# Kernel optimization log

Hardware: AMD Instinct MI355X
Metric: run time of the kernel (lower is better)

Reference implementation:

```python
import jax, jax.numpy as jnp
import numpy as np

B, T = 32, 512
IN, D, H, HD, L, FFN = 375, 512, 8, 64, 6, 1024
NC, CD, LAT, K = 4, 64, 256, 512
DL, DH, DFF, OUT = 4, 512, 1024, 291


def setup_inputs() -> dict:
    key = jax.random.key(0)
    ks = iter(jax.random.split(key, 64))
    def p(shape, scale=0.02):
        return jax.random.normal(next(ks), shape, jnp.float32) * scale
    return {
        "x": jax.random.normal(next(ks), (B, T, IN), jnp.float32),
        "in_w": p((IN, D)), "in_b": jnp.zeros((D,), jnp.float32),
        "enc_ln1_s": jnp.ones((L, D), jnp.float32), "enc_ln1_b": jnp.zeros((L, D), jnp.float32),
        "enc_qkv_w": p((L, D, 3 * D)), "enc_qkv_b": jnp.zeros((L, 3 * D), jnp.float32),
        "enc_out_w": p((L, D, D)), "enc_out_b": jnp.zeros((L, D), jnp.float32),
        "enc_ln2_s": jnp.ones((L, D), jnp.float32), "enc_ln2_b": jnp.zeros((L, D), jnp.float32),
        "enc_ff1_w": p((L, D, FFN)), "enc_ff1_b": jnp.zeros((L, FFN), jnp.float32),
        "enc_ff2_w": p((L, FFN, D)), "enc_ff2_b": jnp.zeros((L, D), jnp.float32),
        "lat_w": p((D, LAT)), "lat_b": jnp.zeros((LAT,), jnp.float32),
        "codebook": jax.random.uniform(next(ks), (K, CD), jnp.float32, -1.0 / K, 1.0 / K),
        "unlat_w": p((LAT, DH)), "unlat_b": jnp.zeros((DH,), jnp.float32),
        "dec_ln_s": jnp.ones((DL, DH), jnp.float32), "dec_ln_b": jnp.zeros((DL, DH), jnp.float32),
        "dec_ff1_w": p((DL, DH, DFF)), "dec_ff1_b": jnp.zeros((DL, DFF), jnp.float32),
        "dec_ff2_w": p((DL, DFF, DH)), "dec_ff2_b": jnp.zeros((DL, DH), jnp.float32),
        "out_w": p((DH, OUT)), "out_b": jnp.zeros((OUT,), jnp.float32),
    }


def _ln(x, s, b):
    m = x.mean(-1, keepdims=True)
    v = jnp.var(x, axis=-1, keepdims=True)
    return (x - m) / jnp.sqrt(v + 1e-5) * s + b


def _rope(x, cos, sin):
    # interleaved even/odd rotation, matches torch stack(...,-1).flatten(-2)
    xe, xo = x[..., 0::2], x[..., 1::2]
    re = xe * cos - xo * sin
    ro = xe * sin + xo * cos
    return jnp.stack((re, ro), axis=-1).reshape(x.shape)


def _forward(x, in_w, in_b, enc_ln1_s, enc_ln1_b, enc_qkv_w, enc_qkv_b,
             enc_out_w, enc_out_b, enc_ln2_s, enc_ln2_b, enc_ff1_w, enc_ff1_b,
             enc_ff2_w, enc_ff2_b, lat_w, lat_b, codebook, unlat_w, unlat_b,
             dec_ln_s, dec_ln_b, dec_ff1_w, dec_ff1_b, dec_ff2_w, dec_ff2_b,
             out_w, out_b):
    h = x @ in_w + in_b  # [B,T,D]
    inv_freq = 1.0 / (10000.0 ** (jnp.arange(0, HD, 2, dtype=jnp.float32) / HD))
    freqs = jnp.outer(jnp.arange(T, dtype=jnp.float32), inv_freq)  # [T, HD/2]
    cos, sin = jnp.cos(freqs), jnp.sin(freqs)
    for i in range(L):
        y = _ln(h, enc_ln1_s[i], enc_ln1_b[i])
        qkv = (y @ enc_qkv_w[i] + enc_qkv_b[i]).reshape(B, T, 3, H, HD)
        qkv = qkv.transpose(2, 0, 3, 1, 4)  # [3,B,H,T,HD]
        q, k, v = qkv[0], qkv[1], qkv[2]
        q = _rope(q, cos, sin)
        k = _rope(k, cos, sin)
        sc = jnp.einsum('bhqd,bhkd->bhqk', q, k) / np.float32(np.sqrt(HD))
        probs = jax.nn.softmax(sc, axis=-1)
        a = jnp.einsum('bhqk,bhkd->bhqd', probs, v)
        a = a.transpose(0, 2, 1, 3).reshape(B, T, D)
        h = h + (a @ enc_out_w[i] + enc_out_b[i])
        y = _ln(h, enc_ln2_s[i], enc_ln2_b[i])
        h = h + (jax.nn.gelu(y @ enc_ff1_w[i] + enc_ff1_b[i], approximate=False)
                 @ enc_ff2_w[i] + enc_ff2_b[i])
    # VQ bottleneck: split each token latent into NC subvectors, nearest code each
    z_bt = (h @ lat_w + lat_b).reshape(B * T, LAT)
    flat_z = z_bt.reshape(-1, CD)  # [B*T*NC, CD]
    d = ((flat_z ** 2).sum(1, keepdims=True)
         - 2.0 * (flat_z @ codebook.T)
         + (codebook ** 2).sum(1))  # [B*T*NC, K]
    idx = jnp.argmin(d, axis=1)
    q_bt = codebook[idx].reshape(B * T, LAT)
    st = z_bt + jax.lax.stop_gradient(q_bt - z_bt)  # straight-through
    g = st.reshape(B, T, LAT) @ unlat_w + unlat_b
    for i in range(DL):
        y = _ln(g, dec_ln_s[i], dec_ln_b[i])
        g = g + (jax.nn.gelu(y @ dec_ff1_w[i] + dec_ff1_b[i], approximate=False)
                 @ dec_ff2_w[i] + dec_ff2_b[i])
    return g @ out_w + out_b  # [B,T,291]


def reference(x, in_w, in_b, enc_ln1_s, enc_ln1_b, enc_qkv_w, enc_qkv_b,
              enc_out_w, enc_out_b, enc_ln2_s, enc_ln2_b, enc_ff1_w, enc_ff1_b,
              enc_ff2_w, enc_ff2_b, lat_w, lat_b, codebook, unlat_w, unlat_b,
              dec_ln_s, dec_ln_b, dec_ff1_w, dec_ff1_b, dec_ff2_w, dec_ff2_b,
              out_w, out_b):
    return _forward(x, in_w, in_b, enc_ln1_s, enc_ln1_b, enc_qkv_w, enc_qkv_b,
                    enc_out_w, enc_out_b, enc_ln2_s, enc_ln2_b, enc_ff1_w, enc_ff1_b,
                    enc_ff2_w, enc_ff2_b, lat_w, lat_b, codebook, unlat_w, unlat_b,
                    dec_ln_s, dec_ln_b, dec_ff1_w, dec_ff1_b, dec_ff2_w, dec_ff2_b,
                    out_w, out_b)
```

## Files before the change

### kernel.cpp

```cpp
#include <hip/hip_runtime.h>
#include <hip/hip_bf16.h>

#define BB 32
#define TT 512
#define IND 375
#define DD 512
#define HH 8
#define HDD 64
#define LL 6
#define FFNN 1024
#define LATD 256
#define KCODES 512
#define DLL 4
#define DHH 512
#define DFFF 1024
#define OUTD 291
#define MTOK (BB*TT)

__global__ void rope_table_k(float* __restrict__ cosb, float* __restrict__ sinb) {
  int idx = blockIdx.x * blockDim.x + threadIdx.x;
  if (idx >= TT * 32) return;
  int t = idx >> 5, i = idx & 31;
  float inv = powf(10000.0f, -(float)(2 * i) / 64.0f);
  float f = (float)t * inv;
  cosb[idx] = cosf(f);
  sinb[idx] = sinf(f);
}

template<int EPI>
__global__ __launch_bounds__(256) void gemm_k(const float* __restrict__ A,
                                              const float* __restrict__ W,
                                              const float* __restrict__ bias,
                                              const float* __restrict__ R,
                                              float* __restrict__ C,
                                              int M, int K, int N) {
  __shared__ float As[16][65];
  __shared__ float Bs[16][64];
  const int bn = blockIdx.x * 64;
  const int bm = blockIdx.y * 64;
  const int tid = threadIdx.x;
  const int tx = tid & 15, ty = tid >> 4;
  float acc[4][4] = {};

  for (int k0 = 0; k0 < K; k0 += 16) {
    {
      int r = tid >> 2, kk = (tid & 3) << 2;
      int gr = bm + r;
#pragma unroll
      for (int j = 0; j < 4; ++j) {
        int kg = k0 + kk + j;
        As[kk + j][r] = (gr < M && kg < K) ? A[(size_t)gr * K + kg] : 0.0f;
      }
    }
    {
      int kk = tid >> 4, nn = (tid & 15) << 2;
      int kg = k0 + kk;
#pragma unroll
      for (int j = 0; j < 4; ++j) {
        int ng = bn + nn + j;
        Bs[kk][nn + j] = (kg < K && ng < N) ? W[(size_t)kg * N + ng] : 0.0f;
      }
    }
    __syncthreads();
#pragma unroll
    for (int kk = 0; kk < 16; ++kk) {
      float a0[4], b0[4];
#pragma unroll
      for (int j = 0; j < 4; ++j) { a0[j] = As[kk][ty * 4 + j]; b0[j] = Bs[kk][tx * 4 + j]; }
#pragma unroll
      for (int ii = 0; ii < 4; ++ii)
#pragma unroll
        for (int jj = 0; jj < 4; ++jj)
          acc[ii][jj] += a0[ii] * b0[jj];
    }
    __syncthreads();
  }

#pragma unroll
  for (int ii = 0; ii < 4; ++ii) {
    int m = bm + ty * 4 + ii;
    if (m >= M) continue;
#pragma unroll
    for (int jj = 0; jj < 4; ++jj) {
      int n = bn + tx * 4 + jj;
      if (n >= N) continue;
      float v = acc[ii][jj] + bias[n];
      if (EPI == 1) v += R[(size_t)m * N + n];
      if (EPI == 2) v = 0.5f * v * (1.0f + erff(v * 0.70710678118654752f));
      C[(size_t)m * N + n] = v;
    }
  }
}

template<int EPI>
__global__ __launch_bounds__(256) void gemm128_k(const float* __restrict__ A,
                                                 const float* __restrict__ W,
                                                 const float* __restrict__ bias,
                                                 const float* __restrict__ R,
                                                 float* __restrict__ C,
                                                 int M, int K, int N) {
  __shared__ float As[16][128];
  __shared__ float4 Bs4[16][2][16];
  const int bn = blockIdx.x * 128;
  const int bm = blockIdx.y * 128;
  const int tid = threadIdx.x;
  const int tx = tid & 15;
  const int ty = tid >> 4;
  const int ar = tid >> 1;
  const int ak = (tid & 1) * 8;
  const int bk = tid >> 4;
  const int bx = tid & 15;

  float acc[8][8] = {};

  for (int k0 = 0; k0 < K; k0 += 16) {
    const float* ap = A + (size_t)(bm + ar) * K + k0 + ak;
    float4 a0 = *(const float4*)ap;
    float4 a1 = *(const float4*)(ap + 4);
    const float* bp = W + (size_t)(k0 + bk) * N + bn + bx * 8;
    float4 b0 = *(const float4*)bp;
    float4 b1 = *(const float4*)(bp + 4);

    __syncthreads();
    As[ak + 0][ar] = a0.x; As[ak + 1][ar] = a0.y; As[ak + 2][ar] = a0.z; As[ak + 3][ar] = a0.w;
    As[ak + 4][ar] = a1.x; As[ak + 5][ar] = a1.y; As[ak + 6][ar] = a1.z; As[ak + 7][ar] = a1.w;
    Bs4[bk][0][bx] = b0;
    Bs4[bk][1][bx] = b1;
    __syncthreads();

#pragma unroll
    for (int kk = 0; kk < 16; ++kk) {
      float4 va0 = *(const float4*)&As[kk][ty * 8];
      float4 va1 = *(const float4*)&As[kk][ty * 8 + 4];
      float4 vb0 = Bs4[kk][0][tx];
      float4 vb1 = Bs4[kk][1][tx];
      float av[8] = {va0.x, va0.y, va0.z, va0.w, va1.x, va1.y, va1.z, va1.w};
      float bv[8] = {vb0.x, vb0.y, vb0.z, vb0.w, vb1.x, vb1.y, vb1.z, vb1.w};
#pragma unroll
      for (int ii = 0; ii < 8; ++ii)
#pragma unroll
        for (int jj = 0; jj < 8; ++jj)
          acc[ii][jj] = __builtin_fmaf(av[ii], bv[jj], acc[ii][jj]);
    }
  }

#pragma unroll
  for (int ii = 0; ii < 8; ++ii) {
    int m = bm + ty * 8 + ii;
#pragma unroll
    for (int g = 0; g < 2; ++g) {
      int n0 = bn + tx * 8 + g * 4;
      float4 vv;
      float t[4];
#pragma unroll
      for (int j = 0; j < 4; ++j) {
        float v = acc[ii][g * 4 + j] + bias[n0 + j];
        if (EPI == 1) v += R[(size_t)m * N + n0 + j];
        if (EPI == 2) v = 0.5f * v * (1.0f + erff(v * 0.70710678118654752f));
        t[j] = v;
      }
      vv.x = t[0]; vv.y = t[1]; vv.z = t[2]; vv.w = t[3];
      *(float4*)&C[(size_t)m * N + n0] = vv;
    }
  }
}

__global__ __launch_bounds__(256) void ln_k(const float* __restrict__ X,
                                            const float* __restrict__ s,
                                            const float* __restrict__ b,
                                            float* __restrict__ Y) {
  int wave = threadIdx.x >> 6, lane = threadIdx.x & 63;
  int row = blockIdx.x * 4 + wave;
  const float* x = X + (size_t)row * DD;
  float v[8];
  float sum = 0.0f;
#pragma unroll
  for (int j = 0; j < 8; ++j) { v[j] = x[lane + 64 * j]; sum += v[j]; }
#pragma unroll
  for (int o = 32; o; o >>= 1) sum += __shfl_xor(sum, o);
  float mean = sum * (1.0f / 512.0f);
  float var = 0.0f;
#pragma unroll
  for (int j = 0; j < 8; ++j) { float d = v[j] - mean; var += d * d; }
#pragma unroll
  for (int o = 32; o; o >>= 1) var += __shfl_xor(var, o);
  float inv = 1.0f / sqrtf(var * (1.0f / 512.0f) + 1e-5f);
  float* y = Y + (size_t)row * DD;
#pragma unroll
  for (int j = 0; j < 8; ++j) {
    int d = lane + 64 * j;
    y[d] = (v[j] - mean) * inv * s[d] + b[d];
  }
}

__global__ void rope_k(float* __restrict__ qkv, const float* __restrict__ cosb,
                       const float* __restrict__ sinb) {
  int idx = blockIdx.x * blockDim.x + threadIdx.x;
  if (idx >= BB * TT * 2 * HH * 32) return;
  int i = idx & 31; idx >>= 5;
  int h = idx & 7;  idx >>= 3;
  int s = idx & 1;  idx >>= 1;
  int t = idx & 511; idx >>= 9;
  int b = idx;
  size_t base = ((size_t)(b * TT + t)) * (3 * DD) + s * DD + h * HDD + 2 * i;
  float c = cosb[t * 32 + i], sn = sinb[t * 32 + i];
  float xe = qkv[base], xo = qkv[base + 1];
  qkv[base]     = xe * c - xo * sn;
  qkv[base + 1] = xe * sn + xo * c;
}

__global__ __launch_bounds__(256) void fattn_k(const float* __restrict__ qkv,
                                               float* __restrict__ out) {
  __shared__ float Qs[64][68];
  __shared__ float KVs[64][68];
  __shared__ float Ps[64][68];
  const int tid = threadIdx.x;
  const int tx = tid & 15, ty = tid >> 4;
  const int qt = blockIdx.x & 7;
  const int h  = (blockIdx.x >> 3) & 7;
  const int b  = blockIdx.x >> 6;
  const float* base = qkv + (size_t)b * TT * (3 * DD) + h * HDD;

  {
    int r = tid & 63, q0 = tid >> 6;
#pragma unroll
    for (int jj = 0; jj < 4; ++jj) {
      int q = q0 + jj * 4;
      float4 v = *(const float4*)(base + (size_t)(qt * 64 + r) * (3 * DD) + q * 4);
      Qs[q * 4 + 0][r] = v.x; Qs[q * 4 + 1][r] = v.y;
      Qs[q * 4 + 2][r] = v.z; Qs[q * 4 + 3][r] = v.w;
    }
  }

  float o[4][4] = {};
  float m[4] = {-1e30f, -1e30f, -1e30f, -1e30f};
  float l[4] = {0.f, 0.f, 0.f, 0.f};

  for (int kt = 0; kt < 8; ++kt) {
    __syncthreads();
    {
      int r = tid & 63, q0 = tid >> 6;
#pragma unroll
      for (int jj = 0; jj < 4; ++jj) {
        int q = q0 + jj * 4;
        float4 v = *(const float4*)(base + (size_t)(kt * 64 + r) * (3 * DD) + DD + q * 4);
        KVs[q * 4 + 0][r] = v.x; KVs[q * 4 + 1][r] = v.y;
        KVs[q * 4 + 2][r] = v.z; KVs[q * 4 + 3][r] = v.w;
      }
    }
    __syncthreads();

    float s[4][4] = {};
#pragma unroll 4
    for (int d = 0; d < 64; ++d) {
      float4 a4 = *(const float4*)&Qs[d][ty * 4];
      float4 b4 = *(const float4*)&KVs[d][tx * 4];
      float av[4] = {a4.x, a4.y, a4.z, a4.w};
      float bv[4] = {b4.x, b4.y, b4.z, b4.w};
#pragma unroll
      for (int ii = 0; ii < 4; ++ii)
#pragma unroll
        for (int jj = 0; jj < 4; ++jj)
          s[ii][jj] = __builtin_fmaf(av[ii], bv[jj], s[ii][jj]);
    }

#pragma unroll
    for (int i = 0; i < 4; ++i) {
      float mm = fmaxf(fmaxf(s[i][0], s[i][1]), fmaxf(s[i][2], s[i][3])) * 0.125f;
#pragma unroll
      for (int off = 1; off < 16; off <<= 1) mm = fmaxf(mm, __shfl_xor(mm, off));
      float mn = fmaxf(m[i], mm);
      float f = expf(m[i] - mn);
      m[i] = mn;
      float ls = 0.0f;
#pragma unroll
      for (int j = 0; j < 4; ++j) {
        float p = expf(__builtin_fmaf(s[i][j], 0.125f, -mn));
        s[i][j] = p;
        ls += p;
      }
#pragma unroll
      for (int off = 1; off < 16; off <<= 1) ls += __shfl_xor(ls, off);
      l[i] = __builtin_fmaf(l[i], f, ls);
#pragma unroll
      for (int j = 0; j < 4; ++j) o[i][j] *= f;
    }

    __syncthreads();

#pragma unroll
    for (int j = 0; j < 4; ++j) {
      float4 pv; pv.x = s[0][j]; pv.y = s[1][j]; pv.z = s[2][j]; pv.w = s[3][j];
      *(float4*)&Ps[tx * 4 + j][ty * 4] = pv;
    }
#pragma unroll
    for (int ii = 0; ii < 4; ++ii) {
      int e = tid + 256 * ii;
      int c = e >> 4, q = e & 15;
      float4 v = *(const float4*)(base + (size_t)(kt * 64 + c) * (3 * DD) + 2 * DD + q * 4);
      *(float4*)&KVs[c][q * 4] = v;
    }
    __syncthreads();

#pragma unroll 4
    for (int c = 0; c < 64; ++c) {
      float4 a4 = *(const float4*)&Ps[c][ty * 4];
      float4 b4 = *(const float4*)&KVs[c][tx * 4];
      float av[4] = {a4.x, a4.y, a4.z, a4.w};
      float bv[4] = {b4.x, b4.y, b4.z, b4.w};
#pragma unroll
      for (int ii = 0; ii < 4; ++ii)
#pragma unroll
        for (int jj = 0; jj < 4; ++jj)
          o[ii][jj] = __builtin_fmaf(av[ii], bv[jj], o[ii][jj]);
    }
  }

#pragma unroll
  for (int i = 0; i < 4; ++i) {
    float inv = 1.0f / l[i];
    int tok = b * TT + qt * 64 + ty * 4 + i;
    float4 vv;
    vv.x = o[i][0] * inv; vv.y = o[i][1] * inv;
    vv.z = o[i][2] * inv; vv.w = o[i][3] * inv;
    *(float4*)&out[(size_t)tok * DD + h * HDD + tx * 4] = vv;
  }
}

__device__ __forceinline__ float npsumsq64(const float* __restrict__ a) {
  float r0 = __fmul_rn(a[0], a[0]), r1 = __fmul_rn(a[1], a[1]);
  float r2 = __fmul_rn(a[2], a[2]), r3 = __fmul_rn(a[3], a[3]);
  float r4 = __fmul_rn(a[4], a[4]), r5 = __fmul_rn(a[5], a[5]);
  float r6 = __fmul_rn(a[6], a[6]), r7 = __fmul_rn(a[7], a[7]);
#pragma unroll
  for (int i = 8; i < 64; i += 8) {
    r0 = __fadd_rn(r0, __fmul_rn(a[i + 0], a[i + 0]));
    r1 = __fadd_rn(r1, __fmul_rn(a[i + 1], a[i + 1]));
    r2 = __fadd_rn(r2, __fmul_rn(a[i + 2], a[i + 2]));
    r3 = __fadd_rn(r3, __fmul_rn(a[i + 3], a[i + 3]));
    r4 = __fadd_rn(r4, __fmul_rn(a[i + 4], a[i + 4]));
    r5 = __fadd_rn(r5, __fmul_rn(a[i + 5], a[i + 5]));
    r6 = __fadd_rn(r6, __fmul_rn(a[i + 6], a[i + 6]));
    r7 = __fadd_rn(r7, __fmul_rn(a[i + 7], a[i + 7]));
  }
  return __fadd_rn(__fadd_rn(__fadd_rn(r0, r1), __fadd_rn(r2, r3)),
                   __fadd_rn(__fadd_rn(r4, r5), __fadd_rn(r6, r7)));
}

__global__ void vqs2_k(const float* __restrict__ CB, float* __restrict__ S2) {
  int k = blockIdx.x * 256 + threadIdx.x;
  if (k < KCODES) S2[k] = npsumsq64(CB + (size_t)k * 64);
}

__global__ __launch_bounds__(256) void vq32b_k(const float* __restrict__ Z,
                                               const float* __restrict__ CB,
                                               const float* __restrict__ S2,
                                               int* __restrict__ idxOut) {
  __shared__ float zs[16][68];
  __shared__ float cs[64][68];
  __shared__ float s2s[64];
  __shared__ float rv[256];
  __shared__ int   ri[256];
  const int tid = threadIdx.x;
  const int lr = tid >> 4;
  const int sub = tid & 15;
  const int row0 = blockIdx.x * 16;

  {
    int r = tid >> 4, q = tid & 15;
    *(float4*)&zs[r][q * 4] = *(const float4*)(Z + (size_t)(row0 + r) * 64 + q * 4);
  }
  __syncthreads();

  const float S1 = npsumsq64(zs[lr]);

  float bv = 3.4e38f;
  int bi = 0x7fffffff;
  for (int ct = 0; ct < 8; ++ct) {
    __syncthreads();
    for (int e = tid; e < 1024; e += 256) {
      int r = e >> 4, q = e & 15;
      *(float4*)&cs[r][q * 4] = *(const float4*)(CB + (size_t)(ct * 64 + r) * 64 + q * 4);
    }
    if (tid < 64) s2s[tid] = S2[ct * 64 + tid];
    __syncthreads();
#pragma unroll
    for (int cc = 0; cc < 4; ++cc) {
      int kl = cc * 16 + sub;
      float g = 0.0f;
#pragma unroll
      for (int d4 = 0; d4 < 16; ++d4) {
        float4 zf = *(const float4*)&zs[lr][d4 * 4];
        float4 cf = *(const float4*)&cs[kl][d4 * 4];
        g = __builtin_fmaf(zf.x, cf.x, g);
        g = __builtin_fmaf(zf.y, cf.y, g);
        g = __builtin_fmaf(zf.z, cf.z, g);
        g = __builtin_fmaf(zf.w, cf.w, g);
      }
      float d32 = __fadd_rn(__fsub_rn(S1, __fmul_rn(2.0f, g)), s2s[kl]);
      int k = ct * 64 + kl;
      if (d32 < bv || (d32 == bv && k < bi)) { bv = d32; bi = k; }
    }
  }
  rv[tid] = bv; ri[tid] = bi;
  __syncthreads();
  if (sub == 0) {
    float bb = rv[tid]; int ii = ri[tid];
#pragma unroll
    for (int j = 1; j < 16; ++j) {
      float v = rv[tid + j]; int id = ri[tid + j];
      if (v < bb || (v == bb && id < ii)) { bb = v; ii = id; }
    }
    idxOut[row0 + lr] = ii;
  }
}

__global__ void stgather_k(const float* __restrict__ Z, const float* __restrict__ CB,
                           const int* __restrict__ idx, float* __restrict__ Q) {
  int e = blockIdx.x * blockDim.x + threadIdx.x;
  if (e >= MTOK * LATD) return;
  int chunk = e >> 6, d = e & 63;
  int k = idx[chunk] & (KCODES - 1);
  float z = Z[e];
  float c = CB[(size_t)k * 64 + d];
  Q[e] = __fadd_rn(z, __fsub_rn(c, z));
}

static inline dim3 gemm_grid(int M, int N) { return dim3((N + 63) / 64, (M + 63) / 64); }
static inline dim3 g128(int M, int N) { return dim3(N / 128, M / 128); }

extern "C" void kernel_launch(void* const* d_in, const int* in_sizes, int n_in,
                              void* d_out, int out_size, void* d_ws, size_t ws_size,
                              hipStream_t stream) {
  const float* x        = (const float*)d_in[0];
  const float* in_w     = (const float*)d_in[1];
  const float* in_b     = (const float*)d_in[2];
  const float* ln1_s    = (const float*)d_in[3];
  const float* ln1_b    = (const float*)d_in[4];
  const float* qkv_w    = (const float*)d_in[5];
  const float* qkv_b    = (const float*)d_in[6];
  const float* aout_w   = (const float*)d_in[7];
  const float* aout_b   = (const float*)d_in[8];
  const float* ln2_s    = (const float*)d_in[9];
  const float* ln2_b    = (const float*)d_in[10];
  const float* ff1_w    = (const float*)d_in[11];
  const float* ff1_b    = (const float*)d_in[12];
  const float* ff2_w    = (const float*)d_in[13];
  const float* ff2_b    = (const float*)d_in[14];
  const float* lat_w    = (const float*)d_in[15];
  const float* lat_b    = (const float*)d_in[16];
  const float* codebook = (const float*)d_in[17];
  const float* unlat_w  = (const float*)d_in[18];
  const float* unlat_b  = (const float*)d_in[19];
  const float* dln_s    = (const float*)d_in[20];
  const float* dln_b    = (const float*)d_in[21];
  const float* dff1_w   = (const float*)d_in[22];
  const float* dff1_b   = (const float*)d_in[23];
  const float* dff2_w   = (const float*)d_in[24];
  const float* dff2_b   = (const float*)d_in[25];
  const float* ow       = (const float*)d_in[26];
  const float* ob       = (const float*)d_in[27];
  float* out = (float*)d_out;

  float* ws   = (float*)d_ws;
  float* Hb   = ws;
  float* Yb   = Hb + (size_t)MTOK * DD;
  float* QKVb = Yb + (size_t)MTOK * DD;
  float* COSb = QKVb + (size_t)MTOK * 3 * DD;
  float* SINb = COSb + TT * 32;
  int*   IDXb = (int*)(SINb + TT * 32);
  float* S2b  = (float*)(IDXb + MTOK * 4);

  dim3 blk(256);

  rope_table_k<<<(TT * 32 + 255) / 256, blk, 0, stream>>>(COSb, SINb);
  vqs2_k<<<2, blk, 0, stream>>>(codebook, S2b);

  gemm_k<0><<<gemm_grid(MTOK, DD), blk, 0, stream>>>(x, in_w, in_b, nullptr, Hb, MTOK, IND, DD);

  for (int l = 0; l < LL; ++l) {
    ln_k<<<MTOK / 4, blk, 0, stream>>>(Hb, ln1_s + l * DD, ln1_b + l * DD, Yb);
    gemm128_k<0><<<g128(MTOK, 3 * DD), blk, 0, stream>>>(Yb, qkv_w + (size_t)l * DD * 3 * DD,
                                                         qkv_b + l * 3 * DD, nullptr, QKVb,
                                                         MTOK, DD, 3 * DD);
    rope_k<<<(BB * TT * 2 * HH * 32) / 256, blk, 0, stream>>>(QKVb, COSb, SINb);
    fattn_k<<<BB * HH * (TT / 64), blk, 0, stream>>>(QKVb, Yb);
    gemm128_k<1><<<g128(MTOK, DD), blk, 0, stream>>>(Yb, aout_w + (size_t)l * DD * DD,
                                                     aout_b + l * DD, Hb, Hb, MTOK, DD, DD);
    ln_k<<<MTOK / 4, blk, 0, stream>>>(Hb, ln2_s + l * DD, ln2_b + l * DD, Yb);
    gemm128_k<2><<<g128(MTOK, FFNN), blk, 0, stream>>>(Yb, ff1_w + (size_t)l * DD * FFNN,
                                                       ff1_b + l * FFNN, nullptr, QKVb,
                                                       MTOK, DD, FFNN);
    gemm128_k<1><<<g128(MTOK, DD), blk, 0, stream>>>(QKVb, ff2_w + (size_t)l * FFNN * DD,
                                                     ff2_b + l * DD, Hb, Hb, MTOK, FFNN, DD);
  }

  gemm128_k<0><<<g128(MTOK, LATD), blk, 0, stream>>>(Hb, lat_w, lat_b, nullptr, Yb, MTOK, DD, LATD);
  vq32b_k<<<(MTOK * 4) / 16, blk, 0, stream>>>(Yb, codebook, S2b, IDXb);
  stgather_k<<<(MTOK * LATD) / 256, blk, 0, stream>>>(Yb, codebook, IDXb, QKVb);
  gemm128_k<0><<<g128(MTOK, DHH), blk, 0, stream>>>(QKVb, unlat_w, unlat_b, nullptr, Hb, MTOK, LATD, DHH);

  for (int l = 0; l < DLL; ++l) {
    ln_k<<<MTOK / 4, blk, 0, stream>>>(Hb, dln_s + l * DHH, dln_b + l * DHH, Yb);
    gemm128_k<2><<<g128(MTOK, DFFF), blk, 0, stream>>>(Yb, dff1_w + (size_t)l * DHH * DFFF,
                                                       dff1_b + l * DFFF, nullptr, QKVb,
                                                       MTOK, DHH, DFFF);
    gemm128_k<1><<<g128(MTOK, DHH), blk, 0, stream>>>(QKVb, dff2_w + (size_t)l * DFFF * DHH,
                                                      dff2_b + l * DHH, Hb, Hb, MTOK, DFFF, DHH);
  }

  gemm_k<0><<<gemm_grid(MTOK, OUTD), blk, 0, stream>>>(Hb, ow, ob, nullptr, out, MTOK, DD, OUTD);
}
```

Before: 9.342 ms.

## Double-buffer GEMM tiles, fuse RoPE into QKV epilogue, XCD-aware block swizzle

The main fp32 GEMM now double-buffers its shared-memory tiles, prefetching the next K-slice into registers while computing the current one, and uses one sync per step instead of two. It also remaps blocks to a 1D grid with XCD-aware swizzling for L2 locality. RoPE is fused into the QKV GEMM epilogue, removing a separate read-modify-write pass over Q and K. The small 64x64 GEMM used for the ragged input and output projections is replaced by a guarded 128x128 variant. Attention block indexing is remapped so that blocks landing on the same XCD share batch and head. The cost is doubled shared memory per block, which may lower occupancy.

```diff
diff --git a/kernel.cpp b/kernel.cpp
--- a/kernel.cpp
+++ b/kernel.cpp
@@ -28,106 +28,146 @@
 }
 
 template<int EPI>
-__global__ __launch_bounds__(256) void gemm_k(const float* __restrict__ A,
-                                              const float* __restrict__ W,
-                                              const float* __restrict__ bias,
-                                              const float* __restrict__ R,
-                                              float* __restrict__ C,
-                                              int M, int K, int N) {
-  __shared__ float As[16][65];
-  __shared__ float Bs[16][64];
-  const int bn = blockIdx.x * 64;
-  const int bm = blockIdx.y * 64;
-  const int tid = threadIdx.x;
-  const int tx = tid & 15, ty = tid >> 4;
-  float acc[4][4] = {};
-
-  for (int k0 = 0; k0 < K; k0 += 16) {
-    {
-      int r = tid >> 2, kk = (tid & 3) << 2;
-      int gr = bm + r;
-#pragma unroll
-      for (int j = 0; j < 4; ++j) {
-        int kg = k0 + kk + j;
-        As[kk + j][r] = (gr < M && kg < K) ? A[(size_t)gr * K + kg] : 0.0f;
-      }
-    }
-    {
-      int kk = tid >> 4, nn = (tid & 15) << 2;
-      int kg = k0 + kk;
-#pragma unroll
-      for (int j = 0; j < 4; ++j) {
-        int ng = bn + nn + j;
-        Bs[kk][nn + j] = (kg < K && ng < N) ? W[(size_t)kg * N + ng] : 0.0f;
-      }
-    }
-    __syncthreads();
-#pragma unroll
-    for (int kk = 0; kk < 16; ++kk) {
-      float a0[4], b0[4];
-#pragma unroll
-      for (int j = 0; j < 4; ++j) { a0[j] = As[kk][ty * 4 + j]; b0[j] = Bs[kk][tx * 4 + j]; }
-#pragma unroll
-      for (int ii = 0; ii < 4; ++ii)
-#pragma unroll
-        for (int jj = 0; jj < 4; ++jj)
-          acc[ii][jj] += a0[ii] * b0[jj];
-    }
-    __syncthreads();
-  }
-
-#pragma unroll
-  for (int ii = 0; ii < 4; ++ii) {
-    int m = bm + ty * 4 + ii;
-    if (m >= M) continue;
-#pragma unroll
-    for (int jj = 0; jj < 4; ++jj) {
-      int n = bn + tx * 4 + jj;
-      if (n >= N) continue;
-      float v = acc[ii][jj] + bias[n];
-      if (EPI == 1) v += R[(size_t)m * N + n];
-      if (EPI == 2) v = 0.5f * v * (1.0f + erff(v * 0.70710678118654752f));
-      C[(size_t)m * N + n] = v;
-    }
-  }
-}
-
-template<int EPI>
 __global__ __launch_bounds__(256) void gemm128_k(const float* __restrict__ A,
                                                  const float* __restrict__ W,
                                                  const float* __restrict__ bias,
                                                  const float* __restrict__ R,
                                                  float* __restrict__ C,
-                                                 int M, int K, int N) {
+                                                 int M, int K, int N,
+                                                 const float* __restrict__ COS,
+                                                 const float* __restrict__ SIN) {
+  __shared__ float As[2][16][128];
+  __shared__ float4 Bs4[2][16][2][16];
+  const int nbx = N >> 7;
+  const int per = gridDim.x >> 3;
+  const int bid = blockIdx.x;
+  const int lin = (bid & 7) * per + (bid >> 3);
+  const int by = lin / nbx, bx = lin - by * nbx;
+  const int bn = bx * 128, bm = by * 128;
+  const int tid = threadIdx.x;
+  const int tx = tid & 15, ty = tid >> 4;
+  const int ar = tid >> 1, ak = (tid & 1) * 8;
+  const int bk = tid >> 4, bxs = tid & 15;
+
+  const float* ap0 = A + (size_t)(bm + ar) * K + ak;
+  const float* bp0 = W + (size_t)bk * N + bn + bxs * 8;
+
+  float acc[8][8] = {};
+  float4 a0, a1, b0, b1;
+
+  a0 = *(const float4*)ap0;
+  a1 = *(const float4*)(ap0 + 4);
+  b0 = *(const float4*)bp0;
+  b1 = *(const float4*)(bp0 + 4);
+  As[0][ak + 0][ar] = a0.x; As[0][ak + 1][ar] = a0.y; As[0][ak + 2][ar] = a0.z; As[0][ak + 3][ar] = a0.w;
+  As[0][ak + 4][ar] = a1.x; As[0][ak + 5][ar] = a1.y; As[0][ak + 6][ar] = a1.z; As[0][ak + 7][ar] = a1.w;
+  Bs4[0][bk][0][bxs] = b0;
+  Bs4[0][bk][1][bxs] = b1;
+  __syncthreads();
+
+  const int nt = K >> 4;
+  int cur = 0;
+  for (int t = 0; t < nt; ++t) {
+    if (t + 1 < nt) {
+      const float* ap = ap0 + (t + 1) * 16;
+      a0 = *(const float4*)ap;
+      a1 = *(const float4*)(ap + 4);
+      const float* bp = bp0 + (size_t)(t + 1) * 16 * N;
+      b0 = *(const float4*)bp;
+      b1 = *(const float4*)(bp + 4);
+    }
+#pragma unroll
+    for (int kk = 0; kk < 16; ++kk) {
+      float4 va0 = *(const float4*)&As[cur][kk][ty * 8];
+      float4 va1 = *(const float4*)&As[cur][kk][ty * 8 + 4];
+      float4 vb0 = Bs4[cur][kk][0][tx];
+      float4 vb1 = Bs4[cur][kk][1][tx];
+      float av[8] = {va0.x, va0.y, va0.z, va0.w, va1.x, va1.y, va1.z, va1.w};
+      float bv[8] = {vb0.x, vb0.y, vb0.z, vb0.w, vb1.x, vb1.y, vb1.z, vb1.w};
+#pragma unroll
+      for (int ii = 0; ii < 8; ++ii)
+#pragma unroll
+        for (int jj = 0; jj < 8; ++jj)
+          acc[ii][jj] = __builtin_fmaf(av[ii], bv[jj], acc[ii][jj]);
+    }
+    if (t + 1 < nt) {
+      int nx = cur ^ 1;
+      As[nx][ak + 0][ar] = a0.x; As[nx][ak + 1][ar] = a0.y; As[nx][ak + 2][ar] = a0.z; As[nx][ak + 3][ar] = a0.w;
+      As[nx][ak + 4][ar] = a1.x; As[nx][ak + 5][ar] = a1.y; As[nx][ak + 6][ar] = a1.z; As[nx][ak + 7][ar] = a1.w;
+      Bs4[nx][bk][0][bxs] = b0;
+      Bs4[nx][bk][1][bxs] = b1;
+      __syncthreads();
+      cur = nx;
+    }
+  }
+
+#pragma unroll
+  for (int ii = 0; ii < 8; ++ii) {
+    int m = bm + ty * 8 + ii;
+#pragma unroll
+    for (int g = 0; g < 2; ++g) {
+      int n0 = bn + tx * 8 + g * 4;
+      float t4[4];
+#pragma unroll
+      for (int j = 0; j < 4; ++j) {
+        float v = acc[ii][g * 4 + j] + bias[n0 + j];
+        if (EPI == 1) v += R[(size_t)m * N + n0 + j];
+        if (EPI == 2) v = 0.5f * v * (1.0f + erff(v * 0.70710678118654752f));
+        t4[j] = v;
+      }
+      if (EPI == 3 && n0 < 2 * DD) {
+        int tpos = m & 511;
+        int i0 = (n0 & 63) >> 1;
+        float c0 = COS[tpos * 32 + i0],     s0 = SIN[tpos * 32 + i0];
+        float c1 = COS[tpos * 32 + i0 + 1], s1 = SIN[tpos * 32 + i0 + 1];
+        float xe0 = t4[0], xo0 = t4[1], xe1 = t4[2], xo1 = t4[3];
+        t4[0] = xe0 * c0 - xo0 * s0;
+        t4[1] = xe0 * s0 + xo0 * c0;
+        t4[2] = xe1 * c1 - xo1 * s1;
+        t4[3] = xe1 * s1 + xo1 * c1;
+      }
+      float4 vv; vv.x = t4[0]; vv.y = t4[1]; vv.z = t4[2]; vv.w = t4[3];
+      *(float4*)&C[(size_t)m * N + n0] = vv;
+    }
+  }
+}
+
+template<int EPI>
+__global__ __launch_bounds__(256) void gemm128g_k(const float* __restrict__ A,
+                                                  const float* __restrict__ W,
+                                                  const float* __restrict__ bias,
+                                                  const float* __restrict__ R,
+                                                  float* __restrict__ C,
+                                                  int M, int K, int N) {
   __shared__ float As[16][128];
   __shared__ float4 Bs4[16][2][16];
   const int bn = blockIdx.x * 128;
   const int bm = blockIdx.y * 128;
   const int tid = threadIdx.x;
-  const int tx = tid & 15;
-  const int ty = tid >> 4;
-  const int ar = tid >> 1;
-  const int ak = (tid & 1) * 8;
-  const int bk = tid >> 4;
-  const int bx = tid & 15;
-
+  const int tx = tid & 15, ty = tid >> 4;
   float acc[8][8] = {};
-
-  for (int k0 = 0; k0 < K; k0 += 16) {
-    const float* ap = A + (size_t)(bm + ar) * K + k0 + ak;
-    float4 a0 = *(const float4*)ap;
-    float4 a1 = *(const float4*)(ap + 4);
-    const float* bp = W + (size_t)(k0 + bk) * N + bn + bx * 8;
-    float4 b0 = *(const float4*)bp;
-    float4 b1 = *(const float4*)(bp + 4);
-
-    __syncthreads();
-    As[ak + 0][ar] = a0.x; As[ak + 1][ar] = a0.y; As[ak + 2][ar] = a0.z; As[ak + 3][ar] = a0.w;
-    As[ak + 4][ar] = a1.x; As[ak + 5][ar] = a1.y; As[ak + 6][ar] = a1.z; As[ak + 7][ar] = a1.w;
-    Bs4[bk][0][bx] = b0;
-    Bs4[bk][1][bx] = b1;
-    __syncthreads();
-
+  float* Bsf = (float*)Bs4;
+
+  const int nt = (K + 15) >> 4;
+  for (int t = 0; t < nt; ++t) {
+    const int k0 = t * 16;
+    __syncthreads();
+#pragma unroll
+    for (int i = 0; i < 8; ++i) {
+      int e = tid + i * 256;
+      int r = e & 127, kk = e >> 7;
+      int kg = k0 + kk;
+      As[kk][r] = (kg < K) ? A[(size_t)(bm + r) * K + kg] : 0.0f;
+    }
+#pragma unroll
+    for (int i = 0; i < 8; ++i) {
+      int e = tid + i * 256;
+      int n = e & 127, kk = e >> 7;
+      int kg = k0 + kk, ng = bn + n;
+      float w = (kg < K && ng < N) ? W[(size_t)kg * N + ng] : 0.0f;
+      Bsf[kk * 128 + ((n >> 2) & 1) * 64 + (n >> 3) * 4 + (n & 3)] = w;
+    }
+    __syncthreads();
 #pragma unroll
     for (int kk = 0; kk < 16; ++kk) {
       float4 va0 = *(const float4*)&As[kk][ty * 8];
@@ -148,19 +188,13 @@
   for (int ii = 0; ii < 8; ++ii) {
     int m = bm + ty * 8 + ii;
 #pragma unroll
-    for (int g = 0; g < 2; ++g) {
-      int n0 = bn + tx * 8 + g * 4;
-      float4 vv;
-      float t[4];
-#pragma unroll
-      for (int j = 0; j < 4; ++j) {
-        float v = acc[ii][g * 4 + j] + bias[n0 + j];
-        if (EPI == 1) v += R[(size_t)m * N + n0 + j];
-        if (EPI == 2) v = 0.5f * v * (1.0f + erff(v * 0.70710678118654752f));
-        t[j] = v;
-      }
-      vv.x = t[0]; vv.y = t[1]; vv.z = t[2]; vv.w = t[3];
-      *(float4*)&C[(size_t)m * N + n0] = vv;
+    for (int jj = 0; jj < 8; ++jj) {
+      int n = bn + tx * 8 + jj;
+      if (n >= N) continue;
+      float v = acc[ii][jj] + bias[n];
+      if (EPI == 1) v += R[(size_t)m * N + n];
+      if (EPI == 2) v = 0.5f * v * (1.0f + erff(v * 0.70710678118654752f));
+      C[(size_t)m * N + n] = v;
     }
   }
 }
@@ -193,22 +227,6 @@
   }
 }
 
-__global__ void rope_k(float* __restrict__ qkv, const float* __restrict__ cosb,
-                       const float* __restrict__ sinb) {
-  int idx = blockIdx.x * blockDim.x + threadIdx.x;
-  if (idx >= BB * TT * 2 * HH * 32) return;
-  int i = idx & 31; idx >>= 5;
-  int h = idx & 7;  idx >>= 3;
-  int s = idx & 1;  idx >>= 1;
-  int t = idx & 511; idx >>= 9;
-  int b = idx;
-  size_t base = ((size_t)(b * TT + t)) * (3 * DD) + s * DD + h * HDD + 2 * i;
-  float c = cosb[t * 32 + i], sn = sinb[t * 32 + i];
-  float xe = qkv[base], xo = qkv[base + 1];
-  qkv[base]     = xe * c - xo * sn;
-  qkv[base + 1] = xe * sn + xo * c;
-}
-
 __global__ __launch_bounds__(256) void fattn_k(const float* __restrict__ qkv,
                                                float* __restrict__ out) {
   __shared__ float Qs[64][68];
@@ -216,9 +234,12 @@
   __shared__ float Ps[64][68];
   const int tid = threadIdx.x;
   const int tx = tid & 15, ty = tid >> 4;
-  const int qt = blockIdx.x & 7;
-  const int h  = (blockIdx.x >> 3) & 7;
-  const int b  = blockIdx.x >> 6;
+  const int g = blockIdx.x;
+  const int xcd = g & 7, slot = g >> 3;
+  const int qt = slot & 7;
+  const int p = ((slot >> 3) << 3) | xcd;
+  const int h = p & 7;
+  const int b = p >> 3;
   const float* base = qkv + (size_t)b * TT * (3 * DD) + h * HDD;
 
   {
@@ -275,9 +296,9 @@
       float ls = 0.0f;
 #pragma unroll
       for (int j = 0; j < 4; ++j) {
-        float p = expf(__builtin_fmaf(s[i][j], 0.125f, -mn));
-        s[i][j] = p;
-        ls += p;
+        float pp = expf(__builtin_fmaf(s[i][j], 0.125f, -mn));
+        s[i][j] = pp;
+        ls += pp;
       }
 #pragma unroll
       for (int off = 1; off < 16; off <<= 1) ls += __shfl_xor(ls, off);
@@ -426,8 +447,7 @@
   Q[e] = __fadd_rn(z, __fsub_rn(c, z));
 }
 
-static inline dim3 gemm_grid(int M, int N) { return dim3((N + 63) / 64, (M + 63) / 64); }
-static inline dim3 g128(int M, int N) { return dim3(N / 128, M / 128); }
+static inline int g1(int M, int N) { return (M / 128) * (N / 128); }
 
 extern "C" void kernel_launch(void* const* d_in, const int* in_sizes, int n_in,
                               void* d_out, int out_size, void* d_ws, size_t ws_size,
@@ -476,38 +496,42 @@
   rope_table_k<<<(TT * 32 + 255) / 256, blk, 0, stream>>>(COSb, SINb);
   vqs2_k<<<2, blk, 0, stream>>>(codebook, S2b);
 
-  gemm_k<0><<<gemm_grid(MTOK, DD), blk, 0, stream>>>(x, in_w, in_b, nullptr, Hb, MTOK, IND, DD);
+  gemm128g_k<0><<<dim3(4, 128), blk, 0, stream>>>(x, in_w, in_b, nullptr, Hb, MTOK, IND, DD);
 
   for (int l = 0; l < LL; ++l) {
     ln_k<<<MTOK / 4, blk, 0, stream>>>(Hb, ln1_s + l * DD, ln1_b + l * DD, Yb);
-    gemm128_k<0><<<g128(MTOK, 3 * DD), blk, 0, stream>>>(Yb, qkv_w + (size_t)l * DD * 3 * DD,
-                                                         qkv_b + l * 3 * DD, nullptr, QKVb,
-                                                         MTOK, DD, 3 * DD);
-    rope_k<<<(BB * TT * 2 * HH * 32) / 256, blk, 0, stream>>>(QKVb, COSb, SINb);
+    gemm128_k<3><<<g1(MTOK, 3 * DD), blk, 0, stream>>>(Yb, qkv_w + (size_t)l * DD * 3 * DD,
+                                                       qkv_b + l * 3 * DD, nullptr, QKVb,
+                                                       MTOK, DD, 3 * DD, COSb, SINb);
     fattn_k<<<BB * HH * (TT / 64), blk, 0, stream>>>(QKVb, Yb);
-    gemm128_k<1><<<g128(MTOK, DD), blk, 0, stream>>>(Yb, aout_w + (size_t)l * DD * DD,
-                                                     aout_b + l * DD, Hb, Hb, MTOK, DD, DD);
+    gemm128_k<1><<<g1(MTOK, DD), blk, 0, stream>>>(Yb, aout_w + (size_t)l * DD * DD,
+                                                   aout_b + l * DD, Hb, Hb, MTOK, DD, DD,
+                                                   nullptr, nullptr);
     ln_k<<<MTOK / 4, blk, 0, stream>>>(Hb, ln2_s + l * DD, ln2_b + l * DD, Yb);
-    gemm128_k<2><<<g128(MTOK, FFNN), blk, 0, stream>>>(Yb, ff1_w + (size_t)l * DD * FFNN,
-                                                       ff1_b + l * FFNN, nullptr, QKVb,
-                                                       MTOK, DD, FFNN);
-    gemm128_k<1><<<g128(MTOK, DD), blk, 0, stream>>>(QKVb, ff2_w + (size_t)l * FFNN * DD,
-                                                     ff2_b + l * DD, Hb, Hb, MTOK, FFNN, DD);
-  }
-
-  gemm128_k<0><<<g128(MTOK, LATD), blk, 0, stream>>>(Hb, lat_w, lat_b, nullptr, Yb, MTOK, DD, LATD);
+    gemm128_k<2><<<g1(MTOK, FFNN), blk, 0, stream>>>(Yb, ff1_w + (size_t)l * DD * FFNN,
+                                                     ff1_b + l * FFNN, nullptr, QKVb,
+                                                     MTOK, DD, FFNN, nullptr, nullptr);
+    gemm128_k<1><<<g1(MTOK, DD), blk, 0, stream>>>(QKVb, ff2_w + (size_t)l * FFNN * DD,
+                                                   ff2_b + l * DD, Hb, Hb, MTOK, FFNN, DD,
+                                                   nullptr, nullptr);
+  }
+
+  gemm128_k<0><<<g1(MTOK, LATD), blk, 0, stream>>>(Hb, lat_w, lat_b, nullptr, Yb,
+                                                   MTOK, DD, LATD, nullptr, nullptr);
   vq32b_k<<<(MTOK * 4) / 16, blk, 0, stream>>>(Yb, codebook, S2b, IDXb);
   stgather_k<<<(MTOK * LATD) / 256, blk, 0, stream>>>(Yb, codebook, IDXb, QKVb);
-  gemm128_k<0><<<g128(MTOK, DHH), blk, 0, stream>>>(QKVb, unlat_w, unlat_b, nullptr, Hb, MTOK, LATD, DHH);
+  gemm128_k<0><<<g1(MTOK, DHH), blk, 0, stream>>>(QKVb, unlat_w, unlat_b, nullptr, Hb,
+                                                  MTOK, LATD, DHH, nullptr, nullptr);
 
   for (int l = 0; l < DLL; ++l) {
     ln_k<<<MTOK / 4, blk, 0, stream>>>(Hb, dln_s + l * DHH, dln_b + l * DHH, Yb);
-    gemm128_k<2><<<g128(MTOK, DFFF), blk, 0, stream>>>(Yb, dff1_w + (size_t)l * DHH * DFFF,
-                                                       dff1_b + l * DFFF, nullptr, QKVb,
-                                                       MTOK, DHH, DFFF);
-    gemm128_k<1><<<g128(MTOK, DHH), blk, 0, stream>>>(QKVb, dff2_w + (size_t)l * DFFF * DHH,
-                                                      dff2_b + l * DHH, Hb, Hb, MTOK, DFFF, DHH);
-  }
-
-  gemm_k<0><<<gemm_grid(MTOK, OUTD), blk, 0, stream>>>(Hb, ow, ob, nullptr, out, MTOK, DD, OUTD);
-}
+    gemm128_k<2><<<g1(MTOK, DFFF), blk, 0, stream>>>(Yb, dff1_w + (size_t)l * DHH * DFFF,
+                                                     dff1_b + l * DFFF, nullptr, QKVb,
+                                                     MTOK, DHH, DFFF, nullptr, nullptr);
+    gemm128_k<1><<<g1(MTOK, DHH), blk, 0, stream>>>(QKVb, dff2_w + (size_t)l * DFFF * DHH,
+                                                    dff2_b + l * DHH, Hb, Hb, MTOK, DFFF, DHH,
+                                                    nullptr, nullptr);
+  }
+
+  gemm128g_k<0><<<dim3(3, 128), blk, 0, stream>>>(Hb, ow, ob, nullptr, out, MTOK, DHH, OUTD);
+}
```

Result: slower. 11.70 ms (+25.3%).
